# Kernel optimization log

Measured on AMD Instinct MI355X. Metric: run time of the kernel, lower is better.

The kernel has to match this reference:

```python
import jax, jax.numpy as jnp
from jax import lax
import numpy as np

NEG_SLOPE = 0.01  # torch leaky_relu default
KSIZE = 5

def lrelu(x):
    return jax.nn.leaky_relu(x, NEG_SLOPE)

def conv(x, w, b):
    # x: [N,C,H,W], w: [O,I,kh,kw], valid padding (pad=False in ConvChain)
    y = lax.conv_general_dilated(x, w, (1, 1), 'VALID',
                                 dimension_numbers=('NCHW', 'OIHW', 'NCHW'))
    return y + b[None, :, None, None]

def _forward(features, radiance, global_features,
             emb_w0, emb_b0, emb_w, emb_b,
             pf_w0, pf_b0, pf_w1, pf_b1, pf_w2, pf_b2,
             sf_w, sf_b,
             kp_w0, kp_b0, kp_w1, kp_b1, kp_w2, kp_b2):
    bs, spp, nf, h, w = features.shape
    ngf = global_features.shape[1]
    K = KSIZE

    # --- sample_embedding over all samples at once (replaces per-sp loop) ---
    g = jnp.broadcast_to(global_features, (bs, ngf, h, w))
    x = jnp.concatenate(
        [jnp.broadcast_to(g[:, None], (bs, spp, ngf, h, w)), features], axis=2)
    x = x.reshape(bs * spp, ngf + nf, h, w)
    x = lrelu(conv(x, emb_w0, emb_b0))
    for i in range(5):  # hidden conv layers 1..5
        x = lrelu(conv(x, emb_w[i], emb_b[i]))
    x = conv(x, emb_w[5], emb_b[5])  # linear output layer
    pixel_embed = x.reshape(bs, spp, x.shape[1], x.shape[2], x.shape[3]).max(axis=1)

    # --- pixel_features chain (3 layers, last linear) ---
    p = lrelu(conv(pixel_embed, pf_w0, pf_b0))
    p = lrelu(conv(p, pf_w1, pf_b1))
    pfeat = conv(p, pf_w2, pf_b2)  # [bs, pair_width, ph, pw]
    ph, pw = pfeat.shape[2], pfeat.shape[3]

    # --- crop features/radiance so needed = ph + K - 1 ---
    needed = ph + K - 1
    crop = (h - needed) // 2
    feat_c = features[..., crop:crop + needed, crop:crop + needed]
    rad_c = radiance[..., crop:crop + needed, crop:crop + needed]

    # --- gather K*K taps per pixel (unfold) ---
    taps = jnp.stack([feat_c[..., dy:dy + ph, dx:dx + pw]
                      for dy in range(K) for dx in range(K)], axis=0)
    # [K,K,bs,spp,nf,ph,pw] -> [bs,ph,pw,spp,ky,kx,nf]
    taps = taps.reshape(K, K, bs, spp, nf, ph, pw).transpose(2, 5, 6, 3, 0, 1, 4)
    off = jnp.arange(K, dtype=taps.dtype) - K // 2
    taps = taps.at[..., 0].add(off)            # x += kx - K//2 (kx axis)
    taps = taps.at[..., 1].add(off[:, None])   # y += ky - K//2 (ky axis)

    rt = jnp.stack([rad_c[..., dy:dy + ph, dx:dx + pw]
                    for dy in range(K) for dx in range(K)], axis=0)
    # [K,K,bs,spp,3,ph,pw] -> [bs,3,ph,pw,spp,ky,kx]
    rt = rt.reshape(K, K, bs, spp, 3, ph, pw).transpose(2, 4, 5, 6, 3, 0, 1)

    # --- sample_features: single linear layer (FullyConnected depth=1) ---
    sf = jnp.einsum('...f,of->...o', taps, sf_w) + sf_b  # [b,ph,pw,spp,ky,kx,pair]

    # --- kernel_predictor on pixel_features + sample_features ---
    pairf = pfeat.transpose(0, 2, 3, 1)[:, :, :, None, None, None, :]
    hdd = lrelu(jnp.einsum('...i,oi->...o', pairf + sf, kp_w0) + kp_b0)
    hdd = lrelu(jnp.einsum('...i,oi->...o', hdd, kp_w1) + kp_b1)
    wts = (jnp.einsum('...i,oi->...o', hdd, kp_w2) + kp_b2)[..., 0]  # [b,ph,pw,spp,ky,kx]

    # --- weighted radiance accumulate + normalize ---
    unnorm = jnp.einsum('bhwsyx,bchwsyx->bchw', wts, rt)
    sumw = wts.sum(axis=(3, 4, 5))[:, None]  # [b,1,ph,pw]
    return unnorm / (sumw + 1e-8)


def setup_inputs() -> dict:
    key = jax.random.key(0)
    ks = jax.random.split(key, 24)
    BS, SPP, NF, NGF, H, W = 1, 4, 12, 4, 116, 116
    WIDTH, PAIR = 128, 64
    s = 0.05
    inp = {}
    inp['features'] = jax.random.normal(ks[0], (BS, SPP, NF, H, W), jnp.float32)
    inp['radiance'] = jax.random.uniform(ks[1], (BS, SPP, 3, H, W), jnp.float32)
    inp['global_features'] = jax.random.normal(ks[2], (BS, NGF, 1, 1), jnp.float32)
    # sample_embedding: 7 conv layers (first 16->128, rest 128->128, last linear)
    inp['emb_w0'] = jax.random.normal(ks[3], (WIDTH, NF + NGF, 3, 3)) * s
    inp['emb_b0'] = jax.random.normal(ks[4], (WIDTH,)) * s
    inp['emb_w'] = jax.random.normal(ks[5], (6, WIDTH, WIDTH, 3, 3)) * s
    inp['emb_b'] = jax.random.normal(ks[6], (6, WIDTH)) * s
    # pixel_features: 3 conv layers 128->128->128->64 (last linear)
    inp['pf_w0'] = jax.random.normal(ks[7], (WIDTH, WIDTH, 3, 3)) * s
    inp['pf_b0'] = jax.random.normal(ks[8], (WIDTH,)) * s
    inp['pf_w1'] = jax.random.normal(ks[9], (WIDTH, WIDTH, 3, 3)) * s
    inp['pf_b1'] = jax.random.normal(ks[10], (WIDTH,)) * s
    inp['pf_w2'] = jax.random.normal(ks[11], (PAIR, WIDTH, 3, 3)) * s
    inp['pf_b2'] = jax.random.normal(ks[12], (PAIR,)) * s
    # sample_features: FullyConnected(12 -> 64, depth=1) = single linear
    inp['sf_w'] = jax.random.normal(ks[13], (PAIR, NF)) * s
    inp['sf_b'] = jax.random.normal(ks[14], (PAIR,)) * s
    # kernel_predictor: FullyConnected(64 -> 1, depth=3)
    inp['kp_w0'] = jax.random.normal(ks[15], (PAIR, PAIR)) * s
    inp['kp_b0'] = jax.random.normal(ks[16], (PAIR,)) * s
    inp['kp_w1'] = jax.random.normal(ks[17], (PAIR, PAIR)) * s
    inp['kp_b1'] = jax.random.normal(ks[18], (PAIR,)) * s
    inp['kp_w2'] = jax.random.normal(ks[19], (1, PAIR)) * s
    inp['kp_b2'] = jax.random.normal(ks[20], (1,)) * s
    return inp


def reference(features, radiance, global_features,
              emb_w0, emb_b0, emb_w, emb_b,
              pf_w0, pf_b0, pf_w1, pf_b1, pf_w2, pf_b2,
              sf_w, sf_b,
              kp_w0, kp_b0, kp_w1, kp_b1, kp_w2, kp_b2):
    return _forward(features, radiance, global_features,
                    emb_w0, emb_b0, emb_w, emb_b,
                    pf_w0, pf_b0, pf_w1, pf_b1, pf_w2, pf_b2,
                    sf_w, sf_b,
                    kp_w0, kp_b0, kp_w1, kp_b1, kp_w2, kp_b2)
```

## Files before the change

### kernel.cpp

```cpp
#include <hip/hip_runtime.h>


#define HW2 13456
#define NF  12
#define NGF 4

__device__ __forceinline__ float lrelu_f(float x) { return x > 0.f ? x : 0.01f * x; }

__global__ __launch_bounds__(256) void k_buildx0(const float* __restrict__ features,
                                                 const float* __restrict__ gf,
                                                 float* __restrict__ out) {
    int i = blockIdx.x * 256 + threadIdx.x;
    const int total = 4 * 16 * HW2;
    if (i >= total) return;
    int n  = i / (16 * HW2);
    int r  = i - n * (16 * HW2);
    int c  = r / HW2;
    int yx = r - c * HW2;
    float v = (c < NGF) ? gf[c] : features[(n * NF + (c - NGF)) * HW2 + yx];
    out[i] = v;
}

__global__ __launch_bounds__(256) void k_wt(const float* __restrict__ w,
                                            float* __restrict__ wt,
                                            int Cout, int Cin) {
    int i = blockIdx.x * 256 + threadIdx.x;
    int total = Cout * Cin * 9;
    if (i >= total) return;
    int m   = i / (Cin * 9);
    int r   = i - m * (Cin * 9);
    int cin = r / 9;
    int kyx = r - cin * 9;
    wt[(kyx * Cin + cin) * Cout + m] = w[i];
}

__global__ __launch_bounds__(256) void k_wt2(const float* __restrict__ w,
                                             float* __restrict__ wt) {
    int i = blockIdx.x * 256 + threadIdx.x;
    if (i >= 4096) return;
    int o = i >> 6, k = i & 63;
    wt[k * 64 + o] = w[i];
}

template <int CIN, int COUT>
__global__ __launch_bounds__(256) void k_convb(const float* __restrict__ in,
                                               const float* __restrict__ wt,
                                               const float* __restrict__ bias,
                                               float* __restrict__ out,
                                               int H, int W, int relu, int tout) {
    constexpr int MW = COUT / 4;
    const int OH = H - 2, OW = W - 2;
    const int n   = blockIdx.z;
    const int tid = threadIdx.x, lane = tid & 63;
    const int wv  = __builtin_amdgcn_readfirstlane(tid >> 6);
    const int mbase = wv * MW;
    const int lx = lane & 31, lyh = lane >> 5;
    const int ox = blockIdx.x * 32 + lx;
    const int oy = blockIdx.y * 2 + lyh;
    const int cx = min(ox, OW - 1);

    const float* inb = in + (size_t)n * CIN * H * W;
    const int HW = H * W;

    float acc[MW];
    #pragma unroll
    for (int mi = 0; mi < MW; ++mi) acc[mi] = 0.f;

    #pragma unroll
    for (int ky = 0; ky < 3; ++ky) {
        #pragma unroll
        for (int kx = 0; kx < 3; ++kx) {
            const float* ia = inb + (oy + ky) * W + cx + kx;
            const float* wr = wt + (size_t)((ky * 3 + kx) * CIN) * COUT + mbase;
            #pragma unroll 8
            for (int cin = 0; cin < CIN; ++cin) {
                float v = ia[cin * HW];
                const float* w = wr + cin * COUT;
                #pragma unroll
                for (int mi = 0; mi < MW; ++mi)
                    acc[mi] += w[mi] * v;
            }
        }
    }

    if (ox < OW) {
        if (tout) {
            float* ob = out + (size_t)(oy * OW + ox) * COUT;
            #pragma unroll
            for (int mi = 0; mi < MW; ++mi) {
                int m = mbase + mi;
                float val = acc[mi] + bias[m];
                if (relu) val = lrelu_f(val);
                ob[m] = val;
            }
        } else {
            #pragma unroll
            for (int mi = 0; mi < MW; ++mi) {
                int m = mbase + mi;
                float val = acc[mi] + bias[m];
                if (relu) val = lrelu_f(val);
                out[(((size_t)n * COUT + m) * OH + oy) * OW + ox] = val;
            }
        }
    }
}

__global__ __launch_bounds__(256) void k_sppmax(const float* __restrict__ in,
                                                float* __restrict__ out) {
    int i = blockIdx.x * 256 + threadIdx.x;
    const int total = 128 * 102 * 102;
    if (i >= total) return;
    float m = in[i];
    #pragma unroll
    for (int s = 1; s < 4; ++s) m = fmaxf(m, in[i + s * total]);
    out[i] = m;
}

__global__ __launch_bounds__(256) void k_mlp(const float* __restrict__ features,
                                             const float* __restrict__ pfeat_t,
                                             const float* __restrict__ sf_w,
                                             const float* __restrict__ sf_b,
                                             const float* __restrict__ w0t,
                                             const float* __restrict__ b0,
                                             const float* __restrict__ w1t,
                                             const float* __restrict__ b1,
                                             const float* __restrict__ w2, const float* __restrict__ b2,
                                             float* __restrict__ wts) {
    __shared__ float vx[64][256];
    const int t   = threadIdx.x;
    const int gid = blockIdx.x * 256 + t;
    {
        int p  = gid / 100;
        int r  = gid - p * 100;
        int s  = r / 25;
        int tp = r - s * 25;
        int dy = tp / 5;
        int dx = tp - dy * 5;
        int h  = p / 96;
        int w  = p - h * 96;

        int y = 8 + h + dy, x = 8 + w + dx;
        const float* fb = features + (size_t)(s * NF) * HW2 + (size_t)y * 116 + x;
        float f[12];
        #pragma unroll
        for (int i = 0; i < 12; ++i) f[i] = fb[i * HW2];
        f[0] += (float)(dx - 2);
        f[1] += (float)(dy - 2);

        const float* pft = pfeat_t + (size_t)p * 64;
        #pragma unroll
        for (int o = 0; o < 64; ++o) {
            float a = 0.f;
            #pragma unroll
            for (int i = 0; i < 12; ++i) a += sf_w[o * 12 + i] * f[i];
            a += sf_b[o];
            vx[o][t] = pft[o] + a;
        }
    }
    __syncthreads();

    const int lane = t & 63;
    const int og   = 16 * __builtin_amdgcn_readfirstlane(t >> 6);
    const int tl   = lane * 4;

    {
        float acc[16][4];
        #pragma unroll
        for (int j = 0; j < 16; ++j)
            #pragma unroll
            for (int c = 0; c < 4; ++c) acc[j][c] = 0.f;
        #pragma unroll 4
        for (int k = 0; k < 64; ++k) {
            float4 xv = *(const float4*)(&vx[k][tl]);
            const float* wr = w0t + k * 64 + og;
            #pragma unroll
            for (int j = 0; j < 16; ++j) {
                float wj = wr[j];
                acc[j][0] += wj * xv.x; acc[j][1] += wj * xv.y;
                acc[j][2] += wj * xv.z; acc[j][3] += wj * xv.w;
            }
        }
        __syncthreads();
        #pragma unroll
        for (int j = 0; j < 16; ++j) {
            float bj = b0[og + j];
            float4 ov;
            ov.x = lrelu_f(acc[j][0] + bj); ov.y = lrelu_f(acc[j][1] + bj);
            ov.z = lrelu_f(acc[j][2] + bj); ov.w = lrelu_f(acc[j][3] + bj);
            *(float4*)(&vx[og + j][tl]) = ov;
        }
        __syncthreads();
    }

    {
        float acc[16][4];
        #pragma unroll
        for (int j = 0; j < 16; ++j)
            #pragma unroll
            for (int c = 0; c < 4; ++c) acc[j][c] = 0.f;
        #pragma unroll 4
        for (int k = 0; k < 64; ++k) {
            float4 xv = *(const float4*)(&vx[k][tl]);
            const float* wr = w1t + k * 64 + og;
            #pragma unroll
            for (int j = 0; j < 16; ++j) {
                float wj = wr[j];
                acc[j][0] += wj * xv.x; acc[j][1] += wj * xv.y;
                acc[j][2] += wj * xv.z; acc[j][3] += wj * xv.w;
            }
        }
        __syncthreads();
        #pragma unroll
        for (int j = 0; j < 16; ++j) {
            float bj = b1[og + j];
            float4 ov;
            ov.x = lrelu_f(acc[j][0] + bj); ov.y = lrelu_f(acc[j][1] + bj);
            ov.z = lrelu_f(acc[j][2] + bj); ov.w = lrelu_f(acc[j][3] + bj);
            *(float4*)(&vx[og + j][tl]) = ov;
        }
        __syncthreads();
    }

    {
        float a = 0.f;
        #pragma unroll
        for (int i = 0; i < 64; ++i) a += w2[i] * vx[i][t];
        a += b2[0];
        wts[gid] = a;
    }
}

__global__ __launch_bounds__(256) void k_reduce(const float* __restrict__ wts,
                                                const float* __restrict__ radiance,
                                                float* __restrict__ out) {
    int p = blockIdx.x * 256 + threadIdx.x;
    if (p >= 9216) return;
    int h = p / 96, w = p - h * 96;
    float sw = 0.f, un0 = 0.f, un1 = 0.f, un2 = 0.f;
    const float* wp = wts + (size_t)p * 100;
    for (int s = 0; s < 4; ++s) {
        #pragma unroll
        for (int dy = 0; dy < 5; ++dy) {
            #pragma unroll
            for (int dx = 0; dx < 5; ++dx) {
                float wv = wp[s * 25 + dy * 5 + dx];
                sw += wv;
                int y = 8 + h + dy, x = 8 + w + dx;
                const float* rb = radiance + (size_t)(s * 3) * HW2 + (size_t)y * 116 + x;
                un0 += wv * rb[0 * HW2];
                un1 += wv * rb[1 * HW2];
                un2 += wv * rb[2 * HW2];
            }
        }
    }
    float inv = 1.f / (sw + 1e-8f);
    out[0 * 9216 + p] = un0 * inv;
    out[1 * 9216 + p] = un1 * inv;
    out[2 * 9216 + p] = un2 * inv;
}

extern "C" void kernel_launch(void* const* d_in, const int* in_sizes, int n_in,
                              void* d_out, int out_size, void* d_ws, size_t ws_size,
                              hipStream_t stream) {
    const float* features = (const float*)d_in[0];
    const float* radiance = (const float*)d_in[1];
    const float* gf       = (const float*)d_in[2];
    const float* emb_w0   = (const float*)d_in[3];
    const float* emb_b0   = (const float*)d_in[4];
    const float* emb_w    = (const float*)d_in[5];
    const float* emb_b    = (const float*)d_in[6];
    const float* pf_w0    = (const float*)d_in[7];
    const float* pf_b0    = (const float*)d_in[8];
    const float* pf_w1    = (const float*)d_in[9];
    const float* pf_b1    = (const float*)d_in[10];
    const float* pf_w2    = (const float*)d_in[11];
    const float* pf_b2    = (const float*)d_in[12];
    const float* sf_w     = (const float*)d_in[13];
    const float* sf_b     = (const float*)d_in[14];
    const float* kp_w0    = (const float*)d_in[15];
    const float* kp_b0    = (const float*)d_in[16];
    const float* kp_w1    = (const float*)d_in[17];
    const float* kp_b1    = (const float*)d_in[18];
    const float* kp_w2    = (const float*)d_in[19];
    const float* kp_b2    = (const float*)d_in[20];
    float* out = (float*)d_out;

    float* WT = (float*)d_ws;
    float* wt0  = WT;
    float* wtE0 = WT + 18432;
    float* wtP0 = WT + 18432 + 6 * 147456;
    float* wtP1 = WT + 1050624;
    float* wtP2 = WT + 1198080;
    float* w0t  = WT + 1271808;
    float* w1t  = WT + 1275904;
    float* A = WT + 1280000;
    float* B = A + 6653952;

    auto wtr = [&](const float* w, float* dst, int Cout, int Cin) {
        int total = Cout * Cin * 9;
        k_wt<<<dim3((total + 255) / 256), 256, 0, stream>>>(w, dst, Cout, Cin);
    };
    wtr(emb_w0, wt0, 128, 16);
    for (int i = 0; i < 6; ++i) wtr(emb_w + i * 147456, wtE0 + i * 147456, 128, 128);
    wtr(pf_w0, wtP0, 128, 128);
    wtr(pf_w1, wtP1, 128, 128);
    wtr(pf_w2, wtP2, 64, 128);
    k_wt2<<<dim3(16), 256, 0, stream>>>(kp_w0, w0t);
    k_wt2<<<dim3(16), 256, 0, stream>>>(kp_w1, w1t);

    k_buildx0<<<dim3((4 * 16 * HW2 + 255) / 256), 256, 0, stream>>>(features, gf, A);

    auto gridc = [](int H, int W, int N) {
        int OH = H - 2, OW = W - 2;
        return dim3((OW + 31) / 32, OH / 2, N);
    };

    k_convb<16, 128><<<gridc(116, 116, 4), 256, 0, stream>>>(A, wt0, emb_b0, B, 116, 116, 1, 0);
    k_convb<128,128><<<gridc(114, 114, 4), 256, 0, stream>>>(B, wtE0 + 0*147456, emb_b + 0*128, A, 114, 114, 1, 0);
    k_convb<128,128><<<gridc(112, 112, 4), 256, 0, stream>>>(A, wtE0 + 1*147456, emb_b + 1*128, B, 112, 112, 1, 0);
    k_convb<128,128><<<gridc(110, 110, 4), 256, 0, stream>>>(B, wtE0 + 2*147456, emb_b + 2*128, A, 110, 110, 1, 0);
    k_convb<128,128><<<gridc(108, 108, 4), 256, 0, stream>>>(A, wtE0 + 3*147456, emb_b + 3*128, B, 108, 108, 1, 0);
    k_convb<128,128><<<gridc(106, 106, 4), 256, 0, stream>>>(B, wtE0 + 4*147456, emb_b + 4*128, A, 106, 106, 1, 0);
    k_convb<128,128><<<gridc(104, 104, 4), 256, 0, stream>>>(A, wtE0 + 5*147456, emb_b + 5*128, B, 104, 104, 0, 0);

    k_sppmax<<<dim3(1331712 / 256), 256, 0, stream>>>(B, A);

    k_convb<128,128><<<gridc(102, 102, 1), 256, 0, stream>>>(A, wtP0, pf_b0, B, 102, 102, 1, 0);
    k_convb<128,128><<<gridc(100, 100, 1), 256, 0, stream>>>(B, wtP1, pf_b1, A, 100, 100, 1, 0);
    k_convb<128, 64><<<gridc(98,  98,  1), 256, 0, stream>>>(A, wtP2, pf_b2, B, 98,  98,  0, 1);

    k_mlp<<<dim3(3600), 256, 0, stream>>>(features, B, sf_w, sf_b,
                                          w0t, kp_b0, w1t, kp_b1, kp_w2, kp_b2, A);

    k_reduce<<<dim3(36), 256, 0, stream>>>(A, radiance, out);
}
```

Before: 2.452 ms.

## Stage conv weights in LDS per tap and compute two output rows per thread

The direct 3x3 conv kernel now copies each tap's CIN x COUT weight slice into shared memory and reads it with float4 LDS loads, instead of reading weights straight from global memory. Each thread also accumulates two output rows (4 rows per block), so every weight load is reused twice and the grid shrinks. The aim is to cut global and scalar weight-load traffic and raise FMA density. The cost is two block barriers per tap, a 64 KB LDS footprint for 128x128 layers that limits occupancy, and doubled accumulator registers, which risks spills.

```diff
diff --git a/kernel.cpp b/kernel.cpp
--- a/kernel.cpp
+++ b/kernel.cpp
@@ -43,63 +43,86 @@
 }
 
 template <int CIN, int COUT>
-__global__ __launch_bounds__(256) void k_convb(const float* __restrict__ in,
+__global__ __launch_bounds__(256) void k_convl(const float* __restrict__ in,
                                                const float* __restrict__ wt,
                                                const float* __restrict__ bias,
                                                float* __restrict__ out,
                                                int H, int W, int relu, int tout) {
     constexpr int MW = COUT / 4;
+    __shared__ float Wlds[CIN * COUT];
+
     const int OH = H - 2, OW = W - 2;
     const int n   = blockIdx.z;
     const int tid = threadIdx.x, lane = tid & 63;
     const int wv  = __builtin_amdgcn_readfirstlane(tid >> 6);
     const int mbase = wv * MW;
     const int lx = lane & 31, lyh = lane >> 5;
-    const int ox = blockIdx.x * 32 + lx;
-    const int oy = blockIdx.y * 2 + lyh;
-    const int cx = min(ox, OW - 1);
+    const int ox  = blockIdx.x * 32 + lx;
+    const int y0  = blockIdx.y * 4;
+    const int oyA = y0 + lyh, oyB = y0 + 2 + lyh;
+    const int cx  = min(ox, OW - 1);
+    const int cyA = min(oyA, OH - 1), cyB = min(oyB, OH - 1);
 
     const float* inb = in + (size_t)n * CIN * H * W;
     const int HW = H * W;
 
-    float acc[MW];
+    float acc[MW][2];
     #pragma unroll
-    for (int mi = 0; mi < MW; ++mi) acc[mi] = 0.f;
-
-    #pragma unroll
-    for (int ky = 0; ky < 3; ++ky) {
-        #pragma unroll
-        for (int kx = 0; kx < 3; ++kx) {
-            const float* ia = inb + (oy + ky) * W + cx + kx;
-            const float* wr = wt + (size_t)((ky * 3 + kx) * CIN) * COUT + mbase;
-            #pragma unroll 8
-            for (int cin = 0; cin < CIN; ++cin) {
-                float v = ia[cin * HW];
-                const float* w = wr + cin * COUT;
+    for (int mi = 0; mi < MW; ++mi) { acc[mi][0] = 0.f; acc[mi][1] = 0.f; }
+
+    for (int kyx = 0; kyx < 9; ++kyx) {
+        const int ky = kyx / 3, kx = kyx - ky * 3;
+        __syncthreads();
+        {
+            const float* ws = wt + (size_t)kyx * CIN * COUT;
+            #pragma unroll
+            for (int i = 0; i < CIN * COUT / 1024; ++i) {
+                int idx = (i * 256 + tid) * 4;
+                *(float4*)(&Wlds[idx]) = *(const float4*)(&ws[idx]);
+            }
+        }
+        __syncthreads();
+
+        const float* iA = inb + (cyA + ky) * W + cx + kx;
+        const float* iB = inb + (cyB + ky) * W + cx + kx;
+        #pragma unroll 4
+        for (int cin = 0; cin < CIN; ++cin) {
+            float vA = iA[cin * HW];
+            float vB = iB[cin * HW];
+            const int wbase = cin * COUT + mbase;
+            #pragma unroll
+            for (int j = 0; j < MW / 4; ++j) {
+                float4 w4 = *(const float4*)(&Wlds[wbase + 4 * j]);
+                acc[4*j+0][0] += w4.x * vA;  acc[4*j+0][1] += w4.x * vB;
+                acc[4*j+1][0] += w4.y * vA;  acc[4*j+1][1] += w4.y * vB;
+                acc[4*j+2][0] += w4.z * vA;  acc[4*j+2][1] += w4.z * vB;
+                acc[4*j+3][0] += w4.w * vA;  acc[4*j+3][1] += w4.w * vB;
+            }
+        }
+    }
+
+    if (ox < OW) {
+        #pragma unroll
+        for (int p = 0; p < 2; ++p) {
+            int oy = p ? oyB : oyA;
+            if (oy >= OH) continue;
+            if (tout) {
+                float* ob = out + (size_t)(oy * OW + ox) * COUT;
                 #pragma unroll
-                for (int mi = 0; mi < MW; ++mi)
-                    acc[mi] += w[mi] * v;
-            }
-        }
-    }
-
-    if (ox < OW) {
-        if (tout) {
-            float* ob = out + (size_t)(oy * OW + ox) * COUT;
-            #pragma unroll
-            for (int mi = 0; mi < MW; ++mi) {
-                int m = mbase + mi;
-                float val = acc[mi] + bias[m];
-                if (relu) val = lrelu_f(val);
-                ob[m] = val;
-            }
-        } else {
-            #pragma unroll
-            for (int mi = 0; mi < MW; ++mi) {
-                int m = mbase + mi;
-                float val = acc[mi] + bias[m];
-                if (relu) val = lrelu_f(val);
-                out[(((size_t)n * COUT + m) * OH + oy) * OW + ox] = val;
+                for (int mi = 0; mi < MW; ++mi) {
+                    int m = mbase + mi;
+                    float val = acc[mi][p] + bias[m];
+                    if (relu) val = lrelu_f(val);
+                    ob[m] = val;
+                }
+            } else {
+                #pragma unroll
+                for (int mi = 0; mi < MW; ++mi) {
+                    int m = mbase + mi;
+                    float val = acc[mi][p] + bias[m];
+                    if (relu) val = lrelu_f(val);
+                    out[(((size_t)n * COUT + m) * OH + oy) * OW + ox] = val;
+                }
             }
         }
     }
@@ -312,22 +335,22 @@
 
     auto gridc = [](int H, int W, int N) {
         int OH = H - 2, OW = W - 2;
-        return dim3((OW + 31) / 32, OH / 2, N);
+        return dim3((OW + 31) / 32, (OH + 3) / 4, N);
     };
 
-    k_convb<16, 128><<<gridc(116, 116, 4), 256, 0, stream>>>(A, wt0, emb_b0, B, 116, 116, 1, 0);
-    k_convb<128,128><<<gridc(114, 114, 4), 256, 0, stream>>>(B, wtE0 + 0*147456, emb_b + 0*128, A, 114, 114, 1, 0);
-    k_convb<128,128><<<gridc(112, 112, 4), 256, 0, stream>>>(A, wtE0 + 1*147456, emb_b + 1*128, B, 112, 112, 1, 0);
-    k_convb<128,128><<<gridc(110, 110, 4), 256, 0, stream>>>(B, wtE0 + 2*147456, emb_b + 2*128, A, 110, 110, 1, 0);
-    k_convb<128,128><<<gridc(108, 108, 4), 256, 0, stream>>>(A, wtE0 + 3*147456, emb_b + 3*128, B, 108, 108, 1, 0);
-    k_convb<128,128><<<gridc(106, 106, 4), 256, 0, stream>>>(B, wtE0 + 4*147456, emb_b + 4*128, A, 106, 106, 1, 0);
-    k_convb<128,128><<<gridc(104, 104, 4), 256, 0, stream>>>(A, wtE0 + 5*147456, emb_b + 5*128, B, 104, 104, 0, 0);
+    k_convl<16, 128><<<gridc(116, 116, 4), 256, 0, stream>>>(A, wt0, emb_b0, B, 116, 116, 1, 0);
+    k_convl<128,128><<<gridc(114, 114, 4), 256, 0, stream>>>(B, wtE0 + 0*147456, emb_b + 0*128, A, 114, 114, 1, 0);
+    k_convl<128,128><<<gridc(112, 112, 4), 256, 0, stream>>>(A, wtE0 + 1*147456, emb_b + 1*128, B, 112, 112, 1, 0);
+    k_convl<128,128><<<gridc(110, 110, 4), 256, 0, stream>>>(B, wtE0 + 2*147456, emb_b + 2*128, A, 110, 110, 1, 0);
+    k_convl<128,128><<<gridc(108, 108, 4), 256, 0, stream>>>(A, wtE0 + 3*147456, emb_b + 3*128, B, 108, 108, 1, 0);
+    k_convl<128,128><<<gridc(106, 106, 4), 256, 0, stream>>>(B, wtE0 + 4*147456, emb_b + 4*128, A, 106, 106, 1, 0);
+    k_convl<128,128><<<gridc(104, 104, 4), 256, 0, stream>>>(A, wtE0 + 5*147456, emb_b + 5*128, B, 104, 104, 0, 0);
 
     k_sppmax<<<dim3(1331712 / 256), 256, 0, stream>>>(B, A);
 
-    k_convb<128,128><<<gridc(102, 102, 1), 256, 0, stream>>>(A, wtP0, pf_b0, B, 102, 102, 1, 0);
-    k_convb<128,128><<<gridc(100, 100, 1), 256, 0, stream>>>(B, wtP1, pf_b1, A, 100, 100, 1, 0);
-    k_convb<128, 64><<<gridc(98,  98,  1), 256, 0, stream>>>(A, wtP2, pf_b2, B, 98,  98,  0, 1);
+    k_convl<128,128><<<gridc(102, 102, 1), 256, 0, stream>>>(A, wtP0, pf_b0, B, 102, 102, 1, 0);
+    k_convl<128,128><<<gridc(100, 100, 1), 256, 0, stream>>>(B, wtP1, pf_b1, A, 100, 100, 1, 0);
+    k_convl<128, 64><<<gridc(98,  98,  1), 256, 0, stream>>>(A, wtP2, pf_b2, B, 98,  98,  0, 1);
 
     k_mlp<<<dim3(3600), 256, 0, stream>>>(features, B, sf_w, sf_b,
                                           w0t, kp_b0, w1t, kp_b1, kp_w2, kp_b2, A);
```

Measured after the change: 2.607 ms. 1.06x slower.
